# Kernel optimization log

Measured on AMD Instinct MI355X. Metric: run time of the kernel, lower is better.

## Reference

```python
import jax, jax.numpy as jnp
import numpy as np

L, D, H, F = 6, 768, 12, 3072   # layers, d_model, heads, mlp hidden
B, S = 2, 2048                   # batch, seq_len
DH = D // H                      # head dim
EPS = 1e-5


def _layer_norm(x, w, b):
    mu = jnp.mean(x, axis=-1, keepdims=True)
    var = jnp.mean(jnp.square(x - mu), axis=-1, keepdims=True)
    return (x - mu) * jax.lax.rsqrt(var + EPS) * w + b


def setup_inputs() -> dict:
    key = jax.random.key(0)
    ks = jax.random.split(key, 8)
    w = lambda k, shape: jax.random.normal(k, shape, dtype=jnp.float32) * 0.02
    return {
        "x": jax.random.normal(ks[0], (B, S, D), dtype=jnp.float32),
        # attention projections, stacked over layers; weights stored (d_in, d_out)
        "Wq": w(ks[1], (L, D, D)), "bq": jnp.zeros((L, D), jnp.float32),
        "Wk": w(ks[2], (L, D, D)), "bk": jnp.zeros((L, D), jnp.float32),
        "Wv": w(ks[3], (L, D, D)), "bv": jnp.zeros((L, D), jnp.float32),
        "Wo": w(ks[4], (L, D, D)), "bo": jnp.zeros((L, D), jnp.float32),
        "ln1_w": jnp.ones((L, D), jnp.float32), "ln1_b": jnp.zeros((L, D), jnp.float32),
        "W1": w(ks[5], (L, D, F)), "b1": jnp.zeros((L, F), jnp.float32),
        "W2": w(ks[6], (L, F, D)), "b2": jnp.zeros((L, D), jnp.float32),
        "ln2_w": jnp.ones((L, D), jnp.float32), "ln2_b": jnp.zeros((L, D), jnp.float32),
        "lnf_w": jnp.ones((D,), jnp.float32), "lnf_b": jnp.zeros((D,), jnp.float32),
    }


def reference(x, Wq, bq, Wk, bk, Wv, bv, Wo, bo, ln1_w, ln1_b,
              W1, b1, W2, b2, ln2_w, ln2_b, lnf_w, lnf_b):
    scale = DH ** (-0.5)
    for i in range(L):
        # pre-norm MSA block; NB: residual uses the normalized x, as in source
        xn = _layer_norm(x, ln1_w[i], ln1_b[i])
        q = (xn @ Wq[i] + bq[i]).reshape(B, S, H, DH).transpose(0, 2, 1, 3)
        k = (xn @ Wk[i] + bk[i]).reshape(B, S, H, DH).transpose(0, 2, 1, 3)
        v = (xn @ Wv[i] + bv[i]).reshape(B, S, H, DH).transpose(0, 2, 1, 3)
        att = jax.nn.softmax(scale * jnp.einsum('bhqd,bhkd->bhqk', q, k), axis=-1)
        out = jnp.einsum('bhqk,bhkd->bhqd', att, v)
        out = out.transpose(0, 2, 1, 3).reshape(B, S, D)
        x = xn + (out @ Wo[i] + bo[i])
        # pre-norm FFN block; residual uses the normalized x, as in source
        xn2 = _layer_norm(x, ln2_w[i], ln2_b[i])
        h = jax.nn.gelu(xn2 @ W1[i] + b1[i], approximate=False)
        x = xn2 + (h @ W2[i] + b2[i])
    return _layer_norm(x, lnf_w, lnf_b)
```

## Files before the change

### kernel.cpp

```cpp
#include <hip/hip_runtime.h>
#include <stdint.h>

typedef unsigned short u16;
typedef unsigned int   u32;

#define L_N  6
#define D_N  768
#define F_N  3072
#define H_N  12
#define B_N  2
#define S_N  2048
#define BS_N 4096
#define QKV_N 2304
#define CSC  0.18033688011112042f
#define DTHR 11.54f

using bf16x8 = __attribute__((ext_vector_type(8))) short;
using f32x4  = __attribute__((ext_vector_type(4))) float;

__device__ __forceinline__ u16 f2bf(float f) {
  u32 x = __builtin_bit_cast(u32, f);
  x += 0x7FFFu + ((x >> 16) & 1u);
  return (u16)(x >> 16);
}

__device__ __forceinline__ u32 cvt_pk_bf16(float lo, float hi) {
  u32 r;
  asm("v_cvt_pk_bf16_f32 %0, %1, %2" : "=v"(r) : "v"(lo), "v"(hi));
  return r;
}

#define GLOAD16(g, l)                                                                     \
  __builtin_amdgcn_global_load_lds((const __attribute__((address_space(1))) void*)(g),    \
                                   (__attribute__((address_space(3))) void*)(l), 16, 0, 0)

__global__ __launch_bounds__(256) void transpose_cast_kernel(
    const float* __restrict__ in, u16* __restrict__ out, int K, int N,
    size_t out_lstride, int out_rowoff)
{
  __shared__ float tile[32][33];
  const int l  = blockIdx.z;
  const int n0 = blockIdx.x * 32, k0 = blockIdx.y * 32;
  const int tx = threadIdx.x & 31, ty = threadIdx.x >> 5;
  const float* src = in + (size_t)l * K * N;
  u16* dst = out + (size_t)l * out_lstride + (size_t)out_rowoff * K;
#pragma unroll
  for (int i = 0; i < 4; ++i)
    tile[ty + i * 8][tx] = src[(size_t)(k0 + ty + i * 8) * N + n0 + tx];
  __syncthreads();
#pragma unroll
  for (int i = 0; i < 4; ++i)
    dst[(size_t)(n0 + ty + i * 8) * K + k0 + tx] = f2bf(tile[tx][ty + i * 8]);
}

__global__ __launch_bounds__(256) void concat_bias_kernel(
    const float* __restrict__ bq, const float* __restrict__ bk,
    const float* __restrict__ bv, float* __restrict__ out)
{
  const int i = blockIdx.x * 256 + threadIdx.x;
  const int l = i / QKV_N, c = i - l * QKV_N;
  float v = (c < 768) ? bq[l * 768 + c]
          : (c < 1536) ? bk[l * 768 + c - 768]
                       : bv[l * 768 + c - 1536];
  out[i] = v;
}

__global__ __launch_bounds__(256) void ln_kernel(
    const float* __restrict__ x, const float* __restrict__ w, const float* __restrict__ b,
    float* __restrict__ outF, u16* __restrict__ outB)
{
  const int row = blockIdx.x, tid = threadIdx.x;
  const float* xr = x + (size_t)row * D_N;
  float v[3];
  float s = 0.f;
#pragma unroll
  for (int i = 0; i < 3; ++i) { v[i] = xr[tid + i * 256]; s += v[i]; }
  __shared__ float red[8];
  const int wave = tid >> 6, lane = tid & 63;
#pragma unroll
  for (int o = 32; o > 0; o >>= 1) s += __shfl_down(s, o, 64);
  if (lane == 0) red[wave] = s;
  __syncthreads();
  const float mu = (red[0] + red[1] + red[2] + red[3]) * (1.f / D_N);
  float d2 = 0.f;
#pragma unroll
  for (int i = 0; i < 3; ++i) { float d = v[i] - mu; d2 += d * d; }
#pragma unroll
  for (int o = 32; o > 0; o >>= 1) d2 += __shfl_down(d2, o, 64);
  if (lane == 0) red[4 + wave] = d2;
  __syncthreads();
  const float var = (red[4] + red[5] + red[6] + red[7]) * (1.f / D_N);
  const float rs = rsqrtf(var + 1e-5f);
#pragma unroll
  for (int i = 0; i < 3; ++i) {
    const int c = tid + i * 256;
    const float o = (v[i] - mu) * rs * w[c] + b[c];
    if (outF) outF[(size_t)row * D_N + c] = o;
    if (outB) outB[(size_t)row * D_N + c] = f2bf(o);
  }
}

template<bool GELU, bool RES, bool OUTF, bool OUTB, bool SCALEQ>
__global__ __launch_bounds__(256) void gemm_kernel(
    const u16* __restrict__ A, const u16* __restrict__ Wt,
    const float* __restrict__ bias, const float* __restrict__ resid,
    float* __restrict__ outF, u16* __restrict__ outB,
    int M, int N, int K)
{
  __shared__ __align__(16) u16 As[2][128 * 32];
  __shared__ __align__(16) u16 Bs[2][128 * 32];
  const int tid  = threadIdx.x;
  const int wave = tid >> 6, lane = tid & 63;
  const int lr = lane & 15, lg = lane >> 4;
  const int row0 = blockIdx.x * 128, col0 = blockIdx.y * 128;
  const int wr = (wave >> 1) * 64, wc = (wave & 1) * 64;

  const int cb0 = wave * 64;
  const int cb1 = 256 + wave * 64;
  const int r0s = (cb0 + lane) >> 2, c0s = ((cb0 + lane) & 3) << 3;
  const int r1s = (cb1 + lane) >> 2, c1s = ((cb1 + lane) & 3) << 3;

  f32x4 acc[4][4] = {};

#define STAGE(cbuf, kk)                                                           \
  do {                                                                            \
    GLOAD16(A  + (size_t)(row0 + r0s) * K + (kk) + c0s, &As[cbuf][cb0 * 8]);      \
    GLOAD16(Wt + (size_t)(col0 + r0s) * K + (kk) + c0s, &Bs[cbuf][cb0 * 8]);      \
    GLOAD16(A  + (size_t)(row0 + r1s) * K + (kk) + c1s, &As[cbuf][cb1 * 8]);      \
    GLOAD16(Wt + (size_t)(col0 + r1s) * K + (kk) + c1s, &Bs[cbuf][cb1 * 8]);      \
  } while (0)

  STAGE(0, 0);
  __syncthreads();

  int c = 0;
  for (int k0 = 0; k0 < K; k0 += 32, c ^= 1) {
    if (k0 + 32 < K) STAGE(c ^ 1, k0 + 32);
    bf16x8 af[4], bfr[4];
#pragma unroll
    for (int m = 0; m < 4; ++m)
      af[m] = *(const bf16x8*)&As[c][(wr + m * 16 + lr) * 32 + lg * 8];
#pragma unroll
    for (int n = 0; n < 4; ++n)
      bfr[n] = *(const bf16x8*)&Bs[c][(wc + n * 16 + lr) * 32 + lg * 8];
    __builtin_amdgcn_s_setprio(1);
#pragma unroll
    for (int m = 0; m < 4; ++m)
#pragma unroll
      for (int n = 0; n < 4; ++n)
        acc[m][n] = __builtin_amdgcn_mfma_f32_16x16x32_bf16(af[m], bfr[n], acc[m][n], 0, 0, 0);
    __builtin_amdgcn_s_setprio(0);
    __syncthreads();
  }
#undef STAGE

#pragma unroll
  for (int m = 0; m < 4; ++m)
#pragma unroll
    for (int n = 0; n < 4; ++n) {
      const int col = col0 + wc + n * 16 + lr;
      const float bv = bias[col];
#pragma unroll
      for (int r = 0; r < 4; ++r) {
        const int row = row0 + wr + m * 16 + lg * 4 + r;
        float v = acc[m][n][r] + bv;
        if (GELU) v = 0.5f * v * (1.f + erff(v * 0.70710678118f));
        if (SCALEQ && col < 768) v *= CSC;
        const size_t idx = (size_t)row * N + col;
        if (RES)  v += resid[idx];
        if (OUTF) outF[idx] = v;
        if (OUTB) outB[idx] = f2bf(v);
      }
    }
}

__global__ __launch_bounds__(256) void gemm64_kernel(
    const u16* __restrict__ A, const u16* __restrict__ Wt,
    const float* __restrict__ bias, const float* __restrict__ resid,
    float* __restrict__ outF, int M, int N, int K)
{
  __shared__ __align__(16) u16 As[2][64 * 32];
  __shared__ __align__(16) u16 Bs[2][64 * 32];
  const int tid  = threadIdx.x;
  const int wave = tid >> 6, lane = tid & 63;
  const int lr = lane & 15, lg = lane >> 4;
  const int row0 = blockIdx.x * 64, col0 = blockIdx.y * 64;
  const int wr = (wave >> 1) * 32, wc = (wave & 1) * 32;

  const int cb = wave * 64;
  const int ch = cb + lane;
  const int rs = ch >> 2, cs = (ch & 3) << 3;

  f32x4 acc[2][2] = {};

#define STAGE64(cbuf, kk)                                                         \
  do {                                                                            \
    GLOAD16(A  + (size_t)(row0 + rs) * K + (kk) + cs, &As[cbuf][cb * 8]);         \
    GLOAD16(Wt + (size_t)(col0 + rs) * K + (kk) + cs, &Bs[cbuf][cb * 8]);         \
  } while (0)

  STAGE64(0, 0);
  __syncthreads();

  int c = 0;
  for (int k0 = 0; k0 < K; k0 += 32, c ^= 1) {
    if (k0 + 32 < K) STAGE64(c ^ 1, k0 + 32);
    bf16x8 af[2], bfr[2];
#pragma unroll
    for (int m = 0; m < 2; ++m)
      af[m] = *(const bf16x8*)&As[c][(wr + m * 16 + lr) * 32 + lg * 8];
#pragma unroll
    for (int n = 0; n < 2; ++n)
      bfr[n] = *(const bf16x8*)&Bs[c][(wc + n * 16 + lr) * 32 + lg * 8];
    __builtin_amdgcn_s_setprio(1);
#pragma unroll
    for (int m = 0; m < 2; ++m)
#pragma unroll
      for (int n = 0; n < 2; ++n)
        acc[m][n] = __builtin_amdgcn_mfma_f32_16x16x32_bf16(af[m], bfr[n], acc[m][n], 0, 0, 0);
    __builtin_amdgcn_s_setprio(0);
    __syncthreads();
  }
#undef STAGE64

#pragma unroll
  for (int m = 0; m < 2; ++m)
#pragma unroll
    for (int n = 0; n < 2; ++n) {
      const int col = col0 + wc + n * 16 + lr;
      const float bv = bias[col];
#pragma unroll
      for (int r = 0; r < 4; ++r) {
        const int row = row0 + wr + m * 16 + lg * 4 + r;
        const size_t idx = (size_t)row * N + col;
        outF[idx] = acc[m][n][r] + bv + resid[idx];
      }
    }
}

__global__ __launch_bounds__(256) void attn_kernel(
    const u16* __restrict__ QKV, u16* __restrict__ O)
{
  constexpr int LDQ = QKV_N;
  constexpr int NT  = S_N / 64;
  __shared__ __align__(16) u16 Ks [64 * 72];
  __shared__ __align__(16) u16 VTs[64 * 72];
  __shared__ __align__(16) u16 Ps [64 * 72];
  const int tid  = threadIdx.x;
  const int wave = tid >> 6, lane = tid & 63;
  const int lr = lane & 15, lg = lane >> 4;
  const int bh = blockIdx.y;
  const int b = bh / H_N, h = bh - b * H_N;
  const int q0 = blockIdx.x * 64;
  const size_t rowbase = (size_t)b * S_N * LDQ;
  const u16* Qg = QKV + rowbase + h * 64;
  const u16* Kg = QKV + rowbase + 768 + h * 64;
  const u16* Vg = QKV + rowbase + 1536 + h * 64;

  const int qrow = q0 + wave * 16 + lr;
  const bf16x8 qf0 = *(const bf16x8*)(Qg + (size_t)qrow * LDQ + lg * 8);
  const bf16x8 qf1 = *(const bf16x8*)(Qg + (size_t)qrow * LDQ + 32 + lg * 8);

  f32x4 o_acc[4] = {};
  float m = -1e30f, l = 0.f;

  const int kr = tid >> 2, kc = (tid & 3) * 16;
  const int pp = tid >> 3, cg = tid & 7;

  const u16* gk = Kg + (size_t)kr * LDQ + kc;
  const u16* gv = Vg + (size_t)(2 * pp) * LDQ + cg * 8;
  uint4 nk0 = *(const uint4*)gk, nk1 = *(const uint4*)(gk + 8);
  uint4 nv0 = *(const uint4*)gv, nv1 = *(const uint4*)(gv + LDQ);

  for (int t = 0; t < NT; ++t) {
    __syncthreads();
    {
      *(uint4*)&Ks[kr * 72 + kc]     = nk0;
      *(uint4*)&Ks[kr * 72 + kc + 8] = nk1;
      const u16* a0 = (const u16*)&nv0;
      const u16* a1 = (const u16*)&nv1;
#pragma unroll
      for (int j = 0; j < 8; ++j) {
        const int jj = (j + cg) & 7;
        *(u32*)&VTs[(cg * 8 + jj) * 72 + 2 * pp] = (u32)a0[jj] | ((u32)a1[jj] << 16);
      }
    }
    __syncthreads();

    if (t + 1 < NT) {
      const u16* gk1 = Kg + (size_t)((t + 1) * 64 + kr) * LDQ + kc;
      const u16* gv1 = Vg + (size_t)((t + 1) * 64 + 2 * pp) * LDQ + cg * 8;
      nk0 = *(const uint4*)gk1; nk1 = *(const uint4*)(gk1 + 8);
      nv0 = *(const uint4*)gv1; nv1 = *(const uint4*)(gv1 + LDQ);
    }

    f32x4 sv[4];
    __builtin_amdgcn_s_setprio(1);
#pragma unroll
    for (int kt = 0; kt < 4; ++kt) {
      const bf16x8 k0 = *(const bf16x8*)&Ks[(kt * 16 + lr) * 72 + lg * 8];
      const bf16x8 k1 = *(const bf16x8*)&Ks[(kt * 16 + lr) * 72 + 32 + lg * 8];
      f32x4 z4 = {};
      z4 = __builtin_amdgcn_mfma_f32_16x16x32_bf16(k0, qf0, z4, 0, 0, 0);
      z4 = __builtin_amdgcn_mfma_f32_16x16x32_bf16(k1, qf1, z4, 0, 0, 0);
      sv[kt] = z4;
    }
    __builtin_amdgcn_s_setprio(0);

    float mx = sv[0][0];
#pragma unroll
    for (int kt = 0; kt < 4; ++kt)
#pragma unroll
      for (int r = 0; r < 4; ++r) mx = fmaxf(mx, sv[kt][r]);
    mx = fmaxf(mx, __shfl_xor(mx, 16, 64));
    mx = fmaxf(mx, __shfl_xor(mx, 32, 64));
    if (!__all(mx - m <= DTHR)) {
      const float mn = fmaxf(m, mx);
      const float al = __builtin_amdgcn_exp2f(m - mn);
      m = mn;
      l *= al;
#pragma unroll
      for (int dt = 0; dt < 4; ++dt)
#pragma unroll
        for (int r = 0; r < 4; ++r) o_acc[dt][r] *= al;
    }
    float rs = 0.f;
#pragma unroll
    for (int kt = 0; kt < 4; ++kt)
#pragma unroll
      for (int r = 0; r < 4; ++r) {
        const float e = __builtin_amdgcn_exp2f(sv[kt][r] - m);
        sv[kt][r] = e;
        rs += e;
      }
    rs += __shfl_xor(rs, 16, 64);
    rs += __shfl_xor(rs, 32, 64);
    l += rs;

    u16* prow = &Ps[(wave * 16 + lr) * 72];
#pragma unroll
    for (int kt = 0; kt < 4; ++kt) {
      *(u32*)(prow + kt * 16 + lg * 4)     = cvt_pk_bf16(sv[kt][0], sv[kt][1]);
      *(u32*)(prow + kt * 16 + lg * 4 + 2) = cvt_pk_bf16(sv[kt][2], sv[kt][3]);
    }
    const bf16x8 pa0 = *(const bf16x8*)(prow + lg * 8);
    const bf16x8 pa1 = *(const bf16x8*)(prow + 32 + lg * 8);
    __builtin_amdgcn_s_setprio(1);
#pragma unroll
    for (int dt = 0; dt < 4; ++dt) {
      const bf16x8 w0 = *(const bf16x8*)&VTs[(dt * 16 + lr) * 72 + lg * 8];
      const bf16x8 w1 = *(const bf16x8*)&VTs[(dt * 16 + lr) * 72 + 32 + lg * 8];
      o_acc[dt] = __builtin_amdgcn_mfma_f32_16x16x32_bf16(w0, pa0, o_acc[dt], 0, 0, 0);
      o_acc[dt] = __builtin_amdgcn_mfma_f32_16x16x32_bf16(w1, pa1, o_acc[dt], 0, 0, 0);
    }
    __builtin_amdgcn_s_setprio(0);
  }

  const float inv = 1.f / l;
  u16* orow = O + (size_t)(b * S_N + qrow) * D_N + h * 64;
#pragma unroll
  for (int dt = 0; dt < 4; ++dt) {
    *(u32*)(orow + dt * 16 + lg * 4)     = cvt_pk_bf16(o_acc[dt][0] * inv, o_acc[dt][1] * inv);
    *(u32*)(orow + dt * 16 + lg * 4 + 2) = cvt_pk_bf16(o_acc[dt][2] * inv, o_acc[dt][3] * inv);
  }
}

extern "C" void kernel_launch(void* const* d_in, const int* in_sizes, int n_in,
                              void* d_out, int out_size, void* d_ws, size_t ws_size,
                              hipStream_t stream)
{
  (void)in_sizes; (void)n_in; (void)out_size; (void)ws_size;
  const float* x0   = (const float*)d_in[0];
  const float* Wq   = (const float*)d_in[1];
  const float* bq   = (const float*)d_in[2];
  const float* Wk   = (const float*)d_in[3];
  const float* bk   = (const float*)d_in[4];
  const float* Wv   = (const float*)d_in[5];
  const float* bv   = (const float*)d_in[6];
  const float* Wo   = (const float*)d_in[7];
  const float* bo   = (const float*)d_in[8];
  const float* ln1w = (const float*)d_in[9];
  const float* ln1b = (const float*)d_in[10];
  const float* W1   = (const float*)d_in[11];
  const float* b1   = (const float*)d_in[12];
  const float* W2   = (const float*)d_in[13];
  const float* b2   = (const float*)d_in[14];
  const float* ln2w = (const float*)d_in[15];
  const float* ln2b = (const float*)d_in[16];
  const float* lnfw = (const float*)d_in[17];
  const float* lnfb = (const float*)d_in[18];

  char* ws = (char*)d_ws;
  size_t off = 0;
  auto alloc = [&](size_t bytes) {
    char* p = ws + off; off += (bytes + 255) & ~(size_t)255; return p;
  };
  u16*   wqkv_t = (u16*)alloc((size_t)L_N * QKV_N * D_N * 2);
  u16*   wo_t   = (u16*)alloc((size_t)L_N * D_N * D_N * 2);
  u16*   w1_t   = (u16*)alloc((size_t)L_N * D_N * F_N * 2);
  u16*   w2_t   = (u16*)alloc((size_t)L_N * D_N * F_N * 2);
  float* bqkv   = (float*)alloc((size_t)L_N * QKV_N * 4);
  float* x_f    = (float*)alloc((size_t)BS_N * D_N * 4);
  float* xn_f   = (float*)alloc((size_t)BS_N * D_N * 4);
  u16*   xn_b   = (u16*)alloc((size_t)BS_N * D_N * 2);
  u16*   qkvb   = (u16*)alloc((size_t)BS_N * QKV_N * 2);
  u16*   ab     = (u16*)alloc((size_t)BS_N * D_N * 2);
  u16*   hb     = (u16*)alloc((size_t)BS_N * F_N * 2);

  const size_t dd = (size_t)D_N * D_N, qs = (size_t)QKV_N * D_N, df = (size_t)D_N * F_N;
  transpose_cast_kernel<<<dim3(D_N/32, D_N/32, L_N), 256, 0, stream>>>(Wq, wqkv_t, D_N, D_N, qs, 0);
  transpose_cast_kernel<<<dim3(D_N/32, D_N/32, L_N), 256, 0, stream>>>(Wk, wqkv_t, D_N, D_N, qs, 768);
  transpose_cast_kernel<<<dim3(D_N/32, D_N/32, L_N), 256, 0, stream>>>(Wv, wqkv_t, D_N, D_N, qs, 1536);
  transpose_cast_kernel<<<dim3(D_N/32, D_N/32, L_N), 256, 0, stream>>>(Wo, wo_t, D_N, D_N, dd, 0);
  transpose_cast_kernel<<<dim3(F_N/32, D_N/32, L_N), 256, 0, stream>>>(W1, w1_t, D_N, F_N, df, 0);
  transpose_cast_kernel<<<dim3(D_N/32, F_N/32, L_N), 256, 0, stream>>>(W2, w2_t, F_N, D_N, df, 0);
  concat_bias_kernel<<<(L_N * QKV_N) / 256, 256, 0, stream>>>(bq, bk, bv, bqkv);

  const dim3 gQKV(BS_N / 128, QKV_N / 128);
  const dim3 gF  (BS_N / 128, F_N / 128);
  const dim3 g64 (BS_N / 64,  D_N / 64);
  const dim3 gA  (S_N / 64, B_N * H_N);

  const float* xin = x0;
  for (int i = 0; i < L_N; ++i) {
    ln_kernel<<<BS_N, 256, 0, stream>>>(xin, ln1w + i * D_N, ln1b + i * D_N, xn_f, xn_b);
    gemm_kernel<false,false,false,true,true><<<gQKV, 256, 0, stream>>>(
        xn_b, wqkv_t + (size_t)i * qs, bqkv + (size_t)i * QKV_N, nullptr,
        nullptr, qkvb, BS_N, QKV_N, D_N);
    attn_kernel<<<gA, 256, 0, stream>>>(qkvb, ab);
    gemm64_kernel<<<g64, 256, 0, stream>>>(
        ab, wo_t + (size_t)i * dd, bo + i * D_N, xn_f, x_f, BS_N, D_N, D_N);
    ln_kernel<<<BS_N, 256, 0, stream>>>(x_f, ln2w + i * D_N, ln2b + i * D_N, xn_f, xn_b);
    gemm_kernel<true,false,false,true,false><<<gF, 256, 0, stream>>>(
        xn_b, w1_t + (size_t)i * df, b1 + i * F_N, nullptr, nullptr, hb, BS_N, F_N, D_N);
    gemm64_kernel<<<g64, 256, 0, stream>>>(
        hb, w2_t + (size_t)i * df, b2 + i * D_N, xn_f, x_f, BS_N, D_N, F_N);
    xin = x_f;
  }
  ln_kernel<<<BS_N, 256, 0, stream>>>(x_f, lnfw, lnfb, (float*)d_out, nullptr);
}
```

Measured before the change: 1.412 ms.

## Use 32x32x16 MFMA in attention with 128-query blocks and register-resident P

Rewrites the attention kernel to use 32x32x16 bf16 MFMA instructions, with each wave handling 32 query rows, so a block covers 128 queries and the grid along the sequence is halved. The probability tile no longer goes through LDS: it is repacked to bf16 in registers using permlane32_swap and fed directly as the B operand of the PV MFMA. Row max and sum reductions also use permlane32_swap instead of two xor shuffles. This halves K/V reloads per query and removes the P round trip through shared memory, at the cost of more accumulator registers and fewer blocks in the grid.

Result: no change. 1.403 ms (-0.6%).

```diff
diff --git a/kernel.cpp b/kernel.cpp
--- a/kernel.cpp
+++ b/kernel.cpp
@@ -17,6 +17,8 @@
 
 using bf16x8 = __attribute__((ext_vector_type(8))) short;
 using f32x4  = __attribute__((ext_vector_type(4))) float;
+using f32x16 = __attribute__((ext_vector_type(16))) float;
+using u32x2  = __attribute__((ext_vector_type(2))) unsigned int;
 
 __device__ __forceinline__ u16 f2bf(float f) {
   u32 x = __builtin_bit_cast(u32, f);
@@ -245,32 +247,33 @@
   constexpr int NT  = S_N / 64;
   __shared__ __align__(16) u16 Ks [64 * 72];
   __shared__ __align__(16) u16 VTs[64 * 72];
-  __shared__ __align__(16) u16 Ps [64 * 72];
   const int tid  = threadIdx.x;
   const int wave = tid >> 6, lane = tid & 63;
-  const int lr = lane & 15, lg = lane >> 4;
+  const int l31 = lane & 31, l5 = lane >> 5;
   const int bh = blockIdx.y;
   const int b = bh / H_N, h = bh - b * H_N;
-  const int q0 = blockIdx.x * 64;
+  const int q0 = blockIdx.x * 128;
   const size_t rowbase = (size_t)b * S_N * LDQ;
   const u16* Qg = QKV + rowbase + h * 64;
   const u16* Kg = QKV + rowbase + 768 + h * 64;
   const u16* Vg = QKV + rowbase + 1536 + h * 64;
 
-  const int qrow = q0 + wave * 16 + lr;
-  const bf16x8 qf0 = *(const bf16x8*)(Qg + (size_t)qrow * LDQ + lg * 8);
-  const bf16x8 qf1 = *(const bf16x8*)(Qg + (size_t)qrow * LDQ + 32 + lg * 8);
-
-  f32x4 o_acc[4] = {};
+  const int qrow = q0 + wave * 32 + l31;
+  bf16x8 qf[4];
+#pragma unroll
+  for (int ks = 0; ks < 4; ++ks)
+    qf[ks] = *(const bf16x8*)(Qg + (size_t)qrow * LDQ + ks * 16 + l5 * 8);
+
+  f32x16 o0 = {}, o1 = {};
   float m = -1e30f, l = 0.f;
 
   const int kr = tid >> 2, kc = (tid & 3) * 16;
   const int pp = tid >> 3, cg = tid & 7;
 
-  const u16* gk = Kg + (size_t)kr * LDQ + kc;
-  const u16* gv = Vg + (size_t)(2 * pp) * LDQ + cg * 8;
-  uint4 nk0 = *(const uint4*)gk, nk1 = *(const uint4*)(gk + 8);
-  uint4 nv0 = *(const uint4*)gv, nv1 = *(const uint4*)(gv + LDQ);
+  const u16* gk0 = Kg + (size_t)kr * LDQ + kc;
+  const u16* gv0 = Vg + (size_t)(2 * pp) * LDQ + cg * 8;
+  uint4 nk0 = *(const uint4*)gk0, nk1 = *(const uint4*)(gk0 + 8);
+  uint4 nv0 = *(const uint4*)gv0, nv1 = *(const uint4*)(gv0 + LDQ);
 
   for (int t = 0; t < NT; ++t) {
     __syncthreads();
@@ -294,64 +297,78 @@
       nv0 = *(const uint4*)gv1; nv1 = *(const uint4*)(gv1 + LDQ);
     }
 
-    f32x4 sv[4];
+    f32x16 sv0 = {}, sv1 = {};
     __builtin_amdgcn_s_setprio(1);
 #pragma unroll
-    for (int kt = 0; kt < 4; ++kt) {
-      const bf16x8 k0 = *(const bf16x8*)&Ks[(kt * 16 + lr) * 72 + lg * 8];
-      const bf16x8 k1 = *(const bf16x8*)&Ks[(kt * 16 + lr) * 72 + 32 + lg * 8];
-      f32x4 z4 = {};
-      z4 = __builtin_amdgcn_mfma_f32_16x16x32_bf16(k0, qf0, z4, 0, 0, 0);
-      z4 = __builtin_amdgcn_mfma_f32_16x16x32_bf16(k1, qf1, z4, 0, 0, 0);
-      sv[kt] = z4;
+    for (int ks = 0; ks < 4; ++ks) {
+      const bf16x8 kf0 = *(const bf16x8*)&Ks[(l31)      * 72 + ks * 16 + l5 * 8];
+      const bf16x8 kf1 = *(const bf16x8*)&Ks[(32 + l31) * 72 + ks * 16 + l5 * 8];
+      sv0 = __builtin_amdgcn_mfma_f32_32x32x16_bf16(kf0, qf[ks], sv0, 0, 0, 0);
+      sv1 = __builtin_amdgcn_mfma_f32_32x32x16_bf16(kf1, qf[ks], sv1, 0, 0, 0);
     }
     __builtin_amdgcn_s_setprio(0);
 
-    float mx = sv[0][0];
-#pragma unroll
-    for (int kt = 0; kt < 4; ++kt)
-#pragma unroll
-      for (int r = 0; r < 4; ++r) mx = fmaxf(mx, sv[kt][r]);
-    mx = fmaxf(mx, __shfl_xor(mx, 16, 64));
-    mx = fmaxf(mx, __shfl_xor(mx, 32, 64));
+    float mx = sv0[0];
+#pragma unroll
+    for (int i = 0; i < 16; ++i) mx = fmaxf(mx, sv0[i]);
+#pragma unroll
+    for (int i = 0; i < 16; ++i) mx = fmaxf(mx, sv1[i]);
+    {
+      const u32 mb = __builtin_bit_cast(u32, mx);
+      const u32x2 rr = __builtin_amdgcn_permlane32_swap(mb, mb, false, false);
+      mx = fmaxf(__builtin_bit_cast(float, rr[0]), __builtin_bit_cast(float, rr[1]));
+    }
     if (!__all(mx - m <= DTHR)) {
       const float mn = fmaxf(m, mx);
       const float al = __builtin_amdgcn_exp2f(m - mn);
       m = mn;
       l *= al;
 #pragma unroll
-      for (int dt = 0; dt < 4; ++dt)
-#pragma unroll
-        for (int r = 0; r < 4; ++r) o_acc[dt][r] *= al;
+      for (int i = 0; i < 16; ++i) { o0[i] *= al; o1[i] *= al; }
     }
     float rs = 0.f;
 #pragma unroll
-    for (int kt = 0; kt < 4; ++kt)
-#pragma unroll
-      for (int r = 0; r < 4; ++r) {
-        const float e = __builtin_amdgcn_exp2f(sv[kt][r] - m);
-        sv[kt][r] = e;
-        rs += e;
+    for (int i = 0; i < 16; ++i) {
+      const float e = __builtin_amdgcn_exp2f(sv0[i] - m);
+      sv0[i] = e; rs += e;
+    }
+#pragma unroll
+    for (int i = 0; i < 16; ++i) {
+      const float e = __builtin_amdgcn_exp2f(sv1[i] - m);
+      sv1[i] = e; rs += e;
+    }
+    {
+      const u32 sb = __builtin_bit_cast(u32, rs);
+      const u32x2 rr = __builtin_amdgcn_permlane32_swap(sb, sb, false, false);
+      rs = __builtin_bit_cast(float, rr[0]) + __builtin_bit_cast(float, rr[1]);
+    }
+    l += rs;
+
+    bf16x8 pb[4];
+#pragma unroll
+    for (int kb = 0; kb < 2; ++kb) {
+      const f32x16& p = kb ? sv1 : sv0;
+#pragma unroll
+      for (int half = 0; half < 2; ++half) {
+        const int o8 = half * 8;
+        const u32 a0 = cvt_pk_bf16(p[o8 + 0], p[o8 + 1]);
+        const u32 b0 = cvt_pk_bf16(p[o8 + 4], p[o8 + 5]);
+        const u32 a1 = cvt_pk_bf16(p[o8 + 2], p[o8 + 3]);
+        const u32 b1 = cvt_pk_bf16(p[o8 + 6], p[o8 + 7]);
+        const u32x2 r0 = __builtin_amdgcn_permlane32_swap(a0, b0, false, false);
+        const u32x2 r1 = __builtin_amdgcn_permlane32_swap(a1, b1, false, false);
+        u32 w[4] = { r0[0], r1[0], r0[1], r1[1] };
+        pb[kb * 2 + half] = __builtin_bit_cast(bf16x8, *(const uint4*)w);
       }
-    rs += __shfl_xor(rs, 16, 64);
-    rs += __shfl_xor(rs, 32, 64);
-    l += rs;
-
-    u16* prow = &Ps[(wave * 16 + lr) * 72];
-#pragma unroll
-    for (int kt = 0; kt < 4; ++kt) {
-      *(u32*)(prow + kt * 16 + lg * 4)     = cvt_pk_bf16(sv[kt][0], sv[kt][1]);
-      *(u32*)(prow + kt * 16 + lg * 4 + 2) = cvt_pk_bf16(sv[kt][2], sv[kt][3]);
-    }
-    const bf16x8 pa0 = *(const bf16x8*)(prow + lg * 8);
-    const bf16x8 pa1 = *(const bf16x8*)(prow + 32 + lg * 8);
+    }
+
     __builtin_amdgcn_s_setprio(1);
 #pragma unroll
-    for (int dt = 0; dt < 4; ++dt) {
-      const bf16x8 w0 = *(const bf16x8*)&VTs[(dt * 16 + lr) * 72 + lg * 8];
-      const bf16x8 w1 = *(const bf16x8*)&VTs[(dt * 16 + lr) * 72 + 32 + lg * 8];
-      o_acc[dt] = __builtin_amdgcn_mfma_f32_16x16x32_bf16(w0, pa0, o_acc[dt], 0, 0, 0);
-      o_acc[dt] = __builtin_amdgcn_mfma_f32_16x16x32_bf16(w1, pa1, o_acc[dt], 0, 0, 0);
+    for (int ks2 = 0; ks2 < 4; ++ks2) {
+      const bf16x8 vf0 = *(const bf16x8*)&VTs[(l31)      * 72 + ks2 * 16 + l5 * 8];
+      const bf16x8 vf1 = *(const bf16x8*)&VTs[(32 + l31) * 72 + ks2 * 16 + l5 * 8];
+      o0 = __builtin_amdgcn_mfma_f32_32x32x16_bf16(vf0, pb[ks2], o0, 0, 0, 0);
+      o1 = __builtin_amdgcn_mfma_f32_32x32x16_bf16(vf1, pb[ks2], o1, 0, 0, 0);
     }
     __builtin_amdgcn_s_setprio(0);
   }
@@ -359,9 +376,10 @@
   const float inv = 1.f / l;
   u16* orow = O + (size_t)(b * S_N + qrow) * D_N + h * 64;
 #pragma unroll
-  for (int dt = 0; dt < 4; ++dt) {
-    *(u32*)(orow + dt * 16 + lg * 4)     = cvt_pk_bf16(o_acc[dt][0] * inv, o_acc[dt][1] * inv);
-    *(u32*)(orow + dt * 16 + lg * 4 + 2) = cvt_pk_bf16(o_acc[dt][2] * inv, o_acc[dt][3] * inv);
+  for (int r = 0; r < 16; r += 2) {
+    const int dh = (r & 3) + 8 * (r >> 2) + 4 * l5;
+    *(u32*)(orow + dh)      = cvt_pk_bf16(o0[r] * inv, o0[r + 1] * inv);
+    *(u32*)(orow + dh + 32) = cvt_pk_bf16(o1[r] * inv, o1[r + 1] * inv);
   }
 }
 
@@ -419,7 +437,7 @@
   const dim3 gQKV(BS_N / 128, QKV_N / 128);
   const dim3 gF  (BS_N / 128, F_N / 128);
   const dim3 g64 (BS_N / 64,  D_N / 64);
-  const dim3 gA  (S_N / 64, B_N * H_N);
+  const dim3 gA  (S_N / 128, B_N * H_N);
 
   const float* xin = x0;
   for (int i = 0; i < L_N; ++i) {
```
